# Performance work log

Hardware: AMD Instinct MI355X
Metric: run time of the kernel (lower is better)

Reference implementation:

```python
import jax, jax.numpy as jnp
import numpy as np

N, C, T, H, W = 16, 64, 30, 64, 44
PC = 64
OUT_H, OUT_W = 16, 20
T_RATE, H_RATE, W_RATE = 0.4, 4.0 / 8, 10.0 / 11  # torso
HEAD_H_RATE = 1.0 / 8
EPS = 1e-8


def setup_inputs() -> dict:
    key = jax.random.key(0)
    ks = jax.random.split(key, 8)
    x = jax.random.normal(ks[0], (N, C, T, H, W), jnp.float32)
    param_x = jax.random.normal(ks[1], (N, PC), jnp.float32)
    W1 = jax.random.normal(ks[2], (PC, PC // 2), jnp.float32) * 0.1
    b1 = jnp.zeros((PC // 2,), jnp.float32)
    W2 = jax.random.normal(ks[3], (PC // 2, 7), jnp.float32) * 0.1
    b2 = jnp.zeros((7,), jnp.float32)
    Wf = jax.random.normal(ks[4], (C, C), jnp.float32) * 0.05
    bf = jnp.zeros((C,), jnp.float32)
    return {"x": x, "param_x": param_x, "W1": W1, "b1": b1, "W2": W2, "b2": b2, "Wf": Wf, "bf": bf}


def reference(x, param_x, W1, b1, W2, b2, Wf, bf):
    n, c, t, h, w = x.shape
    dtype = x.dtype
    atten_in_t = t * T_RATE
    atten_in_h = h * H_RATE
    atten_in_w = w * W_RATE
    atten_ratio = atten_in_w / atten_in_h
    aout_h = int(round(OUT_W / atten_ratio))
    anchor_t = int(round(t / 2.0))
    anchor_x = int(round(w / 2.0))
    anchor_y = int(round(atten_in_h / 2.0 + h * HEAD_H_RATE))  # torso anchor

    # --- localization MLP (locator stand-in): param_x -> 7 params per sample ---
    hid = jnp.tanh(param_x @ W1 + b1)
    p = hid @ W2 + b2  # [N, 7]
    dt0, dx0, dy0 = p[:, 0:1], p[:, 1:2], p[:, 2:3]
    log_sigma2, log_delta_t, log_delta, log_gamma = p[:, 3:4], p[:, 4:5], p[:, 5:6], p[:, 6:7]

    dx = jnp.tanh(dx0) * atten_in_w / 2.0 + anchor_x          # [N,1]
    dy = jnp.tanh(dy0) * atten_in_h / 2.0 + anchor_y          # [N,1]
    sigma2 = jnp.exp(log_sigma2)                              # [N,1]
    delta = jnp.exp(log_delta) * W_RATE                      # [N,1]
    gamma = jax.nn.sigmoid(log_gamma)                         # [N,1]

    # --- spatial Gaussian filter banks ---
    gx = jnp.arange(OUT_W, dtype=dtype)
    gy = jnp.arange(aout_h, dtype=dtype)
    mu_x = dx + (gx - OUT_W / 2.0) * delta                    # [N, OUT_W]
    mu_y = dy + (gy - aout_h / 2.0) * delta                   # [N, aout_h]
    a = jnp.arange(w, dtype=dtype)
    b = jnp.arange(h, dtype=dtype)
    s2 = sigma2[:, :, None]                                   # [N,1,1]
    Fx = jnp.exp(-((a - mu_x[:, :, None]) ** 2) / (2.0 * s2))  # [N, OUT_W, W]
    Fy = jnp.exp(-((b - mu_y[:, :, None]) ** 2) / (2.0 * s2))  # [N, aout_h, H]
    Fx = Fx / jnp.maximum(jnp.sum(Fx, -1, keepdims=True), EPS)
    Fy = Fy / jnp.maximum(jnp.sum(Fy, -1, keepdims=True), EPS)

    # --- spatial sampling: Fy @ x @ Fx^T over the (C*T)-folded batch dim ---
    x2 = x.reshape(n, c * t, h, w)
    t1 = jnp.einsum('ndhw,nqw->ndhq', x2, Fx)                 # [N, C*T, H, OUT_W]
    g = jnp.einsum('nph,ndhq->ndpq', Fy, t1)                  # [N, C*T, aout_h, OUT_W]
    pad_t = (OUT_H - aout_h) // 2
    pad_b = OUT_H - pad_t - aout_h
    g = jnp.pad(g, ((0, 0), (0, 0), (pad_t, pad_b), (0, 0)))  # [N, C*T, OUT_H, OUT_W]

    # --- temporal linear resampling (grid_sample, align_corners=True, zero pad) ---
    dt = jnp.tanh(dt0) * atten_in_t / 2.0 + anchor_t          # [N,1]
    delta_t = jnp.exp(log_delta_t) * T_RATE                   # [N,1]
    gt = jnp.arange(t, dtype=dtype)
    mu_t = dt + (gt - t / 2.0) * delta_t                      # [N, T] raw frame positions

    gseq = g.reshape(n, c, t, OUT_H * OUT_W).transpose(0, 1, 3, 2).reshape(n, c * OUT_H * OUT_W, t)
    i0f = jnp.floor(mu_t)
    frac = mu_t - i0f
    i0 = i0f.astype(jnp.int32)
    i1 = i0 + 1

    def gather(idx):
        return jnp.take_along_axis(gseq, jnp.clip(idx, 0, t - 1)[:, None, :], axis=2)

    w0 = jnp.where((i0 >= 0) & (i0 < t), 1.0 - frac, 0.0)[:, None, :]
    w1 = jnp.where((i1 >= 0) & (i1 < t), frac, 0.0)[:, None, :]
    samp = gather(i0) * w0 + gather(i1) * w1                  # [N, C*OUT_H*OUT_W, T]
    out = samp.reshape(n, c, OUT_H, OUT_W, t).transpose(0, 1, 4, 2, 3)  # [N,C,T,OUT_H,OUT_W]

    out = out * gamma.reshape(n, 1, 1, 1, 1)
    # feature extraction: pointwise Conv3d (extractor stand-in)
    out = jnp.einsum('ncthw,oc->nothw', out, Wf) + bf[None, :, None, None, None]

    params = jnp.stack([dt[:, 0], dx[:, 0], dy[:, 0], sigma2[:, 0],
                        delta[:, 0], delta_t[:, 0], gamma[:, 0]], 0)  # [7, N]
    return out, jax.lax.stop_gradient(params)
```

## Files before the change

kernel.cpp:

```cpp
#include <hip/hip_runtime.h>
#include <math.h>

#define NN 16
#define CC 64
#define TT 30
#define HH 64
#define WW 44
#define OUTH 16
#define OUTW 20
#define HW 320

#define FX_OFF    0
#define FY_OFF    14080
#define IDX0_OFF  30464
#define IDX1_OFF  30944
#define TW0_OFF   31424
#define TW1_OFF   31904
#define GAM_OFF   32384
#define RNG_OFF   32400
#define G_OFF     32464

__global__ __launch_bounds__(64) void params_kernel(
    const float* __restrict__ param_x, const float* __restrict__ W1,
    const float* __restrict__ b1, const float* __restrict__ W2,
    const float* __restrict__ b2, float* __restrict__ ws,
    float* __restrict__ params_out) {
  int n = blockIdx.x;
  int tid = threadIdx.x;
  __shared__ float px[64];
  __shared__ float hid[32];
  __shared__ float pv[7];

  px[tid] = param_x[n * 64 + tid];
  __syncthreads();
  if (tid < 32) {
    float s = b1[tid];
    #pragma unroll
    for (int k = 0; k < 64; ++k) s += px[k] * W1[k * 32 + tid];
    hid[tid] = tanhf(s);
  }
  __syncthreads();
  if (tid < 7) {
    float s = b2[tid];
    #pragma unroll
    for (int j = 0; j < 32; ++j) s += hid[j] * W2[j * 7 + tid];
    pv[tid] = s;
  }
  __syncthreads();

  float dt      = tanhf(pv[0]) * 6.0f  + 15.0f;
  float dx      = tanhf(pv[1]) * 20.0f + 22.0f;
  float dy      = tanhf(pv[2]) * 16.0f + 24.0f;
  float sigma2  = expf(pv[3]);
  float delta_t = expf(pv[4]) * 0.4f;
  float delta   = expf(pv[5]) * (10.0f / 11.0f);
  float gamma   = 1.0f / (1.0f + expf(-pv[6]));
  float inv2s2  = 1.0f / (2.0f * sigma2);

  if (tid < 20) {
    float mu = dx + ((float)tid - 10.0f) * delta;
    float vals[44];
    float s = 0.0f;
    #pragma unroll
    for (int w = 0; w < 44; ++w) {
      float d = (float)w - mu;
      float e = expf(-d * d * inv2s2);
      vals[w] = e; s += e;
    }
    float inv = 1.0f / fmaxf(s, 1e-8f);
    float* Fx = ws + FX_OFF + n * (20 * 44) + tid * 44;
    #pragma unroll
    for (int w = 0; w < 44; ++w) Fx[w] = vals[w] * inv;
  }
  if (tid < 16) {
    float mu = dy + ((float)tid - 8.0f) * delta;
    float vals[64];
    float s = 0.0f;
    #pragma unroll
    for (int h = 0; h < 64; ++h) {
      float d = (float)h - mu;
      float e = expf(-d * d * inv2s2);
      vals[h] = e; s += e;
    }
    float inv = 1.0f / fmaxf(s, 1e-8f);
    float* Fy = ws + FY_OFF + n * (16 * 64) + tid * 64;
    #pragma unroll
    for (int h = 0; h < 64; ++h) Fy[h] = vals[h] * inv;
  }
  if (tid < 30) {
    float mu = dt + ((float)tid - 15.0f) * delta_t;
    float i0f = floorf(mu);
    float frac = mu - i0f;
    int i0 = (int)i0f;
    int i1 = i0 + 1;
    float w0 = (i0 >= 0 && i0 < TT) ? (1.0f - frac) : 0.0f;
    float w1 = (i1 >= 0 && i1 < TT) ? frac : 0.0f;
    ((int*)(ws + IDX0_OFF))[n * TT + tid] = min(max(i0, 0), TT - 1);
    ((int*)(ws + IDX1_OFF))[n * TT + tid] = min(max(i1, 0), TT - 1);
    ws[TW0_OFF + n * TT + tid] = w0;
    ws[TW1_OFF + n * TT + tid] = w1;
  }
  if (tid == 0) {
    float R = 7.7459667f * sqrtf(sigma2);
    int wlo = max(0,  (int)floorf(dx - 10.0f * delta - R));
    int whi = min(43, (int)ceilf (dx +  9.0f * delta + R));
    int hlo = max(0,  (int)floorf(dy -  8.0f * delta - R));
    int hhi = min(63, (int)ceilf (dy +  7.0f * delta + R));
    int* rng = (int*)(ws + RNG_OFF) + n * 4;
    rng[0] = wlo & ~3;
    rng[1] = whi | 3;
    rng[2] = hlo & ~3;
    rng[3] = hhi | 3;

    ws[GAM_OFF + n] = gamma;
    params_out[0 * NN + n] = dt;
    params_out[1 * NN + n] = dx;
    params_out[2 * NN + n] = dy;
    params_out[3 * NN + n] = sigma2;
    params_out[4 * NN + n] = delta;
    params_out[5 * NN + n] = delta_t;
    params_out[6 * NN + n] = gamma;
  }
}

__global__ __launch_bounds__(256) void spatial_kernel(
    const float* __restrict__ x, const float* __restrict__ ws,
    float* __restrict__ g) {
  int b = blockIdx.x;
  int n  = b / (TT * 16);
  int r  = b % (TT * 16);
  int t  = r / 16;
  int c0 = (r % 16) * 4;

  int tid  = threadIdx.x;
  int cl   = tid >> 6;
  int lane = tid & 63;

  __shared__ float st1[4 * 20 * 68];
  __shared__ float sFy[16 * 68];

  const int* rng = (const int*)(ws + RNG_OFF) + n * 4;
  int wlo4 = rng[0], whi4 = rng[1], hlo4 = rng[2], hhi4 = rng[3];

  {
    const float4* Fy4 = (const float4*)(ws + FY_OFF + n * (16 * 64));
    float4 v = Fy4[tid];
    int p = tid >> 4, h4 = tid & 15;
    *(float4*)&sFy[p * 68 + h4 * 4] = v;
  }

  int c = c0 + cl;
  bool hact = (lane >= hlo4) && (lane <= hhi4);
  if (hact) {
    const float4* xp =
        (const float4*)(x + ((((size_t)n * CC + c) * TT + t) * HH + lane) * WW);
    int ilo = wlo4 >> 2, ihi = whi4 >> 2;
    float xrow[44];
    #pragma unroll
    for (int i = 0; i < 11; ++i) {
      float4 v;
      if (i >= ilo && i <= ihi) v = xp[i];
      else v = make_float4(0.0f, 0.0f, 0.0f, 0.0f);
      xrow[4 * i + 0] = v.x; xrow[4 * i + 1] = v.y;
      xrow[4 * i + 2] = v.z; xrow[4 * i + 3] = v.w;
    }
    const float* fx = ws + FX_OFF + n * (20 * 44);
    #pragma unroll
    for (int q = 0; q < 20; ++q) {
      float s = 0.0f;
      #pragma unroll
      for (int w = 0; w < 44; ++w) s = fmaf(xrow[w], fx[q * 44 + w], s);
      st1[(cl * 20 + q) * 68 + lane] = s;
    }
  }
  __syncthreads();

  int hh = lane >> 5;
  int pp = (lane >> 2) & 7;
  int qg = lane & 3;
  int hc0 = hlo4 >> 2, hc1 = hhi4 >> 2;

  float o[2][5];
  #pragma unroll
  for (int u = 0; u < 2; ++u)
    #pragma unroll
    for (int j = 0; j < 5; ++j) o[u][j] = 0.0f;

  for (int hcc = hc0 + hh; hcc <= hc1; hcc += 2) {
    float4 fy0 = *(const float4*)&sFy[pp * 68 + hcc * 4];
    float4 fy1 = *(const float4*)&sFy[(pp + 8) * 68 + hcc * 4];
    #pragma unroll
    for (int j = 0; j < 5; ++j) {
      int q = qg * 5 + j;
      float4 tv = *(const float4*)&st1[(cl * 20 + q) * 68 + hcc * 4];
      o[0][j] = fmaf(fy0.x, tv.x,
                fmaf(fy0.y, tv.y, fmaf(fy0.z, tv.z, fmaf(fy0.w, tv.w, o[0][j]))));
      o[1][j] = fmaf(fy1.x, tv.x,
                fmaf(fy1.y, tv.y, fmaf(fy1.z, tv.z, fmaf(fy1.w, tv.w, o[1][j]))));
    }
  }
  #pragma unroll
  for (int u = 0; u < 2; ++u)
    #pragma unroll
    for (int j = 0; j < 5; ++j)
      o[u][j] += __shfl_xor(o[u][j], 32);

  if (hh == 0) {
    float* gout = g + ((size_t)((n * CC + c) * TT + t)) * HW;
    #pragma unroll
    for (int u = 0; u < 2; ++u) {
      int p = pp + u * 8;
      #pragma unroll
      for (int j = 0; j < 5; ++j) gout[p * OUTW + qg * 5 + j] = o[u][j];
    }
  }
}

__global__ __launch_bounds__(256) void output_kernel(
    const float* __restrict__ g, const float* __restrict__ ws,
    const float* __restrict__ Wf, const float* __restrict__ bf,
    float* __restrict__ out) {
  int b = blockIdx.x;
  int n    = b / (TT * 2);
  int r    = b % (TT * 2);
  int tp   = r >> 1;
  int hw0  = (r & 1) * 160;
  int tid  = threadIdx.x;

  __shared__ float sWfT[64 * 65];
  __shared__ float smix[64 * 160];

  #pragma unroll
  for (int i = tid; i < 64 * 64; i += 256) {
    int oc = i >> 6, c = i & 63;
    sWfT[c * 65 + oc] = Wf[i];
  }

  int i0 = ((const int*)(ws + IDX0_OFF))[n * TT + tp];
  int i1 = ((const int*)(ws + IDX1_OFF))[n * TT + tp];
  float w0 = ws[TW0_OFF + n * TT + tp];
  float w1 = ws[TW1_OFF + n * TT + tp];
  float gamma = ws[GAM_OFF + n];

  #pragma unroll
  for (int i4 = tid; i4 < 64 * 40; i4 += 256) {
    int c  = i4 / 40;
    int r4 = i4 - c * 40;
    size_t base = (size_t)(n * CC + c) * TT;
    float4 a  = *(const float4*)(g + (base + i0) * HW + hw0 + r4 * 4);
    float4 bb = *(const float4*)(g + (base + i1) * HW + hw0 + r4 * 4);
    float4 m;
    m.x = gamma * fmaf(w0, a.x, w1 * bb.x);
    m.y = gamma * fmaf(w0, a.y, w1 * bb.y);
    m.z = gamma * fmaf(w0, a.z, w1 * bb.z);
    m.w = gamma * fmaf(w0, a.w, w1 * bb.w);
    *(float4*)&smix[c * 160 + r4 * 4] = m;
  }
  __syncthreads();

  int ocg = tid >> 5;
  int hwg = tid & 31;
  int oc0 = ocg * 8;
  int hwl0 = hwg * 5;
  float acc[8][5];
  #pragma unroll
  for (int u = 0; u < 8; ++u)
    #pragma unroll
    for (int j = 0; j < 5; ++j) acc[u][j] = 0.0f;

  #pragma unroll 4
  for (int c = 0; c < 64; ++c) {
    float4 wv0 = *(const float4*)&sWfT[c * 65 + oc0];
    float4 wv1 = *(const float4*)&sWfT[c * 65 + oc0 + 4];
    float m[5];
    #pragma unroll
    for (int j = 0; j < 5; ++j) m[j] = smix[c * 160 + hwl0 + j];
    float wv[8] = {wv0.x, wv0.y, wv0.z, wv0.w, wv1.x, wv1.y, wv1.z, wv1.w};
    #pragma unroll
    for (int u = 0; u < 8; ++u)
      #pragma unroll
      for (int j = 0; j < 5; ++j) acc[u][j] = fmaf(wv[u], m[j], acc[u][j]);
  }

  #pragma unroll
  for (int u = 0; u < 8; ++u) {
    int oc = oc0 + u;
    float bias = bf[oc];
    float* op = out + (((size_t)n * CC + oc) * TT + tp) * HW + hw0 + hwl0;
    #pragma unroll
    for (int j = 0; j < 5; ++j) op[j] = acc[u][j] + bias;
  }
}

extern "C" void kernel_launch(void* const* d_in, const int* in_sizes, int n_in,
                              void* d_out, int out_size, void* d_ws,
                              size_t ws_size, hipStream_t stream) {
  const float* x       = (const float*)d_in[0];
  const float* param_x = (const float*)d_in[1];
  const float* W1      = (const float*)d_in[2];
  const float* b1      = (const float*)d_in[3];
  const float* W2      = (const float*)d_in[4];
  const float* b2      = (const float*)d_in[5];
  const float* Wf      = (const float*)d_in[6];
  const float* bf      = (const float*)d_in[7];
  float* out = (float*)d_out;
  float* ws  = (float*)d_ws;
  float* params_out = out + (size_t)NN * CC * TT * HW;

  params_kernel<<<NN, 64, 0, stream>>>(param_x, W1, b1, W2, b2, ws, params_out);
  spatial_kernel<<<NN * TT * 16, 256, 0, stream>>>(x, ws, ws + G_OFF);
  output_kernel<<<NN * TT * 2, 256, 0, stream>>>(ws + G_OFF, ws, Wf, bf, out);
}
```

Measured before the change: 508.9 us.

## Transpose Fx and loop only over active W range in spatial stage

Stores the Fx filter bank transposed ([w][q]) so the spatial kernel can stream x row chunks and accumulate 20 outputs per chunk. The loop now runs only over the w-chunks inside the precomputed active range instead of a fully unrolled 44-wide dot product with zero-padded chunks, skipping FMAs for chunks outside the range. Range bounds are made wave-uniform with readfirstlane so filter loads can become scalar loads. In exchange the loop is dynamic rather than fully unrolled, and inactive lanes now execute the FMA loop on zeros.

```diff
diff --git a/kernel.cpp b/kernel.cpp
--- a/kernel.cpp
+++ b/kernel.cpp
@@ -10,7 +10,7 @@
 #define OUTW 20
 #define HW 320
 
-#define FX_OFF    0
+#define FXT_OFF   0
 #define FY_OFF    14080
 #define IDX0_OFF  30464
 #define IDX1_OFF  30944
@@ -68,9 +68,9 @@
       vals[w] = e; s += e;
     }
     float inv = 1.0f / fmaxf(s, 1e-8f);
-    float* Fx = ws + FX_OFF + n * (20 * 44) + tid * 44;
-    #pragma unroll
-    for (int w = 0; w < 44; ++w) Fx[w] = vals[w] * inv;
+    float* FxT = ws + FXT_OFF + n * (44 * 20) + tid;
+    #pragma unroll
+    for (int w = 0; w < 44; ++w) FxT[w * 20] = vals[w] * inv;
   }
   if (tid < 16) {
     float mu = dy + ((float)tid - 8.0f) * delta;
@@ -140,7 +140,10 @@
   __shared__ float sFy[16 * 68];
 
   const int* rng = (const int*)(ws + RNG_OFF) + n * 4;
-  int wlo4 = rng[0], whi4 = rng[1], hlo4 = rng[2], hhi4 = rng[3];
+  int wlo4 = __builtin_amdgcn_readfirstlane(rng[0]);
+  int whi4 = __builtin_amdgcn_readfirstlane(rng[1]);
+  int hlo4 = __builtin_amdgcn_readfirstlane(rng[2]);
+  int hhi4 = __builtin_amdgcn_readfirstlane(rng[3]);
 
   {
     const float4* Fy4 = (const float4*)(ws + FY_OFF + n * (16 * 64));
@@ -151,27 +154,30 @@
 
   int c = c0 + cl;
   bool hact = (lane >= hlo4) && (lane <= hhi4);
+  const float4* xp =
+      (const float4*)(x + ((((size_t)n * CC + c) * TT + t) * HH + lane) * WW);
+  const float* fxt = ws + FXT_OFF + n * (44 * 20);
+
+  float acc[20];
+  #pragma unroll
+  for (int q = 0; q < 20; ++q) acc[q] = 0.0f;
+
+  int ilo = wlo4 >> 2, ihi = whi4 >> 2;
+  for (int i = ilo; i <= ihi; ++i) {
+    float4 v = make_float4(0.0f, 0.0f, 0.0f, 0.0f);
+    if (hact) v = xp[i];
+    float vx[4] = {v.x, v.y, v.z, v.w};
+    const float* fr = fxt + i * 80;
+    #pragma unroll
+    for (int k = 0; k < 4; ++k) {
+      #pragma unroll
+      for (int q = 0; q < 20; ++q)
+        acc[q] = fmaf(vx[k], fr[k * 20 + q], acc[q]);
+    }
+  }
   if (hact) {
-    const float4* xp =
-        (const float4*)(x + ((((size_t)n * CC + c) * TT + t) * HH + lane) * WW);
-    int ilo = wlo4 >> 2, ihi = whi4 >> 2;
-    float xrow[44];
-    #pragma unroll
-    for (int i = 0; i < 11; ++i) {
-      float4 v;
-      if (i >= ilo && i <= ihi) v = xp[i];
-      else v = make_float4(0.0f, 0.0f, 0.0f, 0.0f);
-      xrow[4 * i + 0] = v.x; xrow[4 * i + 1] = v.y;
-      xrow[4 * i + 2] = v.z; xrow[4 * i + 3] = v.w;
-    }
-    const float* fx = ws + FX_OFF + n * (20 * 44);
-    #pragma unroll
-    for (int q = 0; q < 20; ++q) {
-      float s = 0.0f;
-      #pragma unroll
-      for (int w = 0; w < 44; ++w) s = fmaf(xrow[w], fx[q * 44 + w], s);
-      st1[(cl * 20 + q) * 68 + lane] = s;
-    }
+    #pragma unroll
+    for (int q = 0; q < 20; ++q) st1[(cl * 20 + q) * 68 + lane] = acc[q];
   }
   __syncthreads();
 
```

After: 523.6 us. 2.9% more time.
